# Kernel optimization log

Hardware: AMD Instinct MI355X
Metric: run time of the kernel (lower is better)

The kernel has to match this reference:

```python
import jax, jax.numpy as jnp
import numpy as np

CHUNKS = 4
QMAX = 127.0

def fake_quant_int8(t):
    # per-tensor amax calibration -> symmetric int8 fake quant with STE
    amax = jnp.max(jnp.abs(t))
    scale = jnp.maximum(amax, 1e-12) / QMAX
    q = jnp.clip(jnp.round(t / scale), -128.0, 127.0) * scale
    return t + jax.lax.stop_gradient(q - t)

def conv2d(x, w):
    # NCHW x, OIHW w; stride 1, padding 1, dilation 1, groups 1
    return jax.lax.conv_general_dilated(
        x, w, window_strides=(1, 1), padding=((1, 1), (1, 1)),
        dimension_numbers=('NCHW', 'OIHW', 'NCHW'))

def setup_inputs() -> dict:
    key = jax.random.key(0)
    k1, k2, k3 = jax.random.split(key, 3)
    x = jax.random.normal(k1, (8, 256, 128, 128), dtype=jnp.float32)
    weight = jax.random.normal(k2, (512, 256, 3, 3), dtype=jnp.float32) * 0.05
    bias_data = jax.random.normal(k3, (512,), dtype=jnp.float32)
    return {'x': x, 'weight': weight, 'bias_data': bias_data}

def reference(x, weight, bias_data):
    # seg_mode='weight', opt_type='default': input quantized once,
    # weight chunked along out_channels, each chunk quantized separately.
    xq = fake_quant_int8(x)
    out_ch = weight.shape[0]
    csize = out_ch // CHUNKS
    outs = []
    for i in range(CHUNKS):
        w_chunk = weight[i * csize:(i + 1) * csize]
        wq = fake_quant_int8(w_chunk)
        outs.append(conv2d(xq, wq))
    res = jnp.concatenate(outs, axis=1)  # [B, out_ch, H, W]
    return res + bias_data[None, :, None, None]
```

## Files before the change

kernel.cpp:

```cpp
#include <hip/hip_runtime.h>
#include <hip/hip_bf16.h>


typedef int i32x4 __attribute__((ext_vector_type(4)));

__device__ __forceinline__ void llds16(const void* g, void* l) {
    __builtin_amdgcn_global_load_lds(
        (const __attribute__((address_space(1))) void*)g,
        (__attribute__((address_space(3))) void*)l,
        16, 0, 0);
}

__device__ __forceinline__ float f4max(float4 v) {
    return fmaxf(fmaxf(fabsf(v.x), fabsf(v.y)), fmaxf(fabsf(v.z), fabsf(v.w)));
}

__global__ __launch_bounds__(256) void k_amax(const float4* __restrict__ x,
                                              const float4* __restrict__ w4,
                                              float* __restrict__ part) {
    __shared__ float red[4];
    int t = threadIdx.x;
    float m = 0.f;
    if (blockIdx.x < 2048) {
        int tid = blockIdx.x * 256 + t;
        float4 v[16];
#pragma unroll
        for (int k = 0; k < 16; ++k)
            v[k] = x[(size_t)tid + (size_t)k * 524288];
#pragma unroll
        for (int k = 0; k < 16; ++k) m = fmaxf(m, f4max(v[k]));
    } else {
        int b = blockIdx.x - 2048;
        int chunk = b / 288;
        int tid = (b - chunk * 288) * 256 + t;
        m = f4max(w4[(size_t)chunk * 73728 + tid]);
    }
    for (int off = 32; off > 0; off >>= 1) m = fmaxf(m, __shfl_xor(m, off, 64));
    if ((t & 63) == 0) red[t >> 6] = m;
    __syncthreads();
    if (t == 0)
        part[blockIdx.x] = fmaxf(fmaxf(red[0], red[1]), fmaxf(red[2], red[3]));
}

__global__ __launch_bounds__(256) void k_amax2(const float* __restrict__ part,
                                               unsigned* __restrict__ amaxb) {
    __shared__ float red[4];
    int t = threadIdx.x;
    float m = 0.f;
#pragma unroll
    for (int k = 0; k < 8; ++k) m = fmaxf(m, part[t + k * 256]);
    for (int off = 32; off > 0; off >>= 1) m = fmaxf(m, __shfl_xor(m, off, 64));
    if ((t & 63) == 0) red[t >> 6] = m;
    __syncthreads();
    if (t == 0)
        amaxb[0] = __float_as_uint(fmaxf(fmaxf(red[0], red[1]), fmaxf(red[2], red[3])));
    int c = t >> 6, l = t & 63;
    float wm = 0.f;
#pragma unroll
    for (int k = 0; k < 5; ++k) {
        int i = l + k * 64;
        if (i < 288) wm = fmaxf(wm, part[2048 + c * 288 + i]);
    }
    for (int off = 32; off > 0; off >>= 1) wm = fmaxf(wm, __shfl_xor(wm, off, 64));
    if (l == 0) amaxb[1 + c] = __float_as_uint(wm);
}

__global__ __launch_bounds__(256) void k_quant_x(const float* __restrict__ x,
                                                 signed char* __restrict__ qx,
                                                 const unsigned* __restrict__ amaxb) {
    float inv = 127.0f / fmaxf(__uint_as_float(amaxb[0]), 1e-12f);
    int row = blockIdx.x;
    int n = row >> 7, h = row & 127;
    int t = threadIdx.x;
    int w4 = t & 31, cg = t >> 5;
    const float* base = x + (size_t)n * 256 * 16384 + (size_t)h * 128 + w4 * 4;
#pragma unroll
    for (int pp = 0; pp < 2; ++pp) {
        int c0 = pp * 128 + cg * 16;
        float4 v[16];
#pragma unroll
        for (int j = 0; j < 16; ++j)
            v[j] = *(const float4*)(base + (size_t)(c0 + j) * 16384);
#pragma unroll
        for (int i = 0; i < 4; ++i) {
            unsigned wds[4];
#pragma unroll
            for (int jg = 0; jg < 4; ++jg) {
                unsigned u = 0;
#pragma unroll
                for (int jj = 0; jj < 4; ++jj) {
                    float f = (&v[jg * 4 + jj].x)[i];
                    int q = (int)fminf(fmaxf(rintf(f * inv), -128.f), 127.f);
                    u |= ((unsigned)(q & 255)) << (8 * jj);
                }
                wds[jg] = u;
            }
            *(uint4*)&qx[(size_t)row * 32768 + (size_t)(w4 * 4 + i) * 256 + c0] =
                make_uint4(wds[0], wds[1], wds[2], wds[3]);
        }
    }
}

__global__ void k_quant_w(const float* __restrict__ wsrc, signed char* __restrict__ qw,
                          const unsigned* __restrict__ amaxb) {
    int idx = blockIdx.x * 256 + threadIdx.x;
    int oc = idx >> 8, c = idx & 255;
    float inv = 127.0f / fmaxf(__uint_as_float(amaxb[1 + (oc >> 7)]), 1e-12f);
    const float* src = wsrc + (size_t)idx * 9;
    float v[9];
#pragma unroll
    for (int rs = 0; rs < 9; ++rs) v[rs] = src[rs];
#pragma unroll
    for (int rs = 0; rs < 9; ++rs) {
        float qf = fminf(fmaxf(rintf(v[rs] * inv), -128.f), 127.f);
        qw[((size_t)(rs * 512 + oc)) * 256 + c] = (signed char)(int)qf;
    }
}

__global__ __launch_bounds__(256, 2) void k_conv(
    const signed char* __restrict__ qx, const signed char* __restrict__ qw,
    const signed char* __restrict__ zb, const unsigned* __restrict__ amaxb,
    const float* __restrict__ bias, float* __restrict__ out) {
    __shared__ __align__(16) signed char xs[4 * 8320];
    __shared__ __align__(16) signed char wt[3 * 128 * 64];
    int orig = blockIdx.x;
    int wgid = (orig & 7) * 256 + (orig >> 3);
    int rowpair = wgid >> 2, ocg = wgid & 3;
    int n = rowpair >> 6;
    int h0 = (rowpair & 63) * 2;
    int t = threadIdx.x, wid = t >> 6, lane = t & 63;
    int lp = lane & 15, hi = lane >> 4;
    int rowsel = wid >> 1, whalf = wid & 1;

    i32x4 acc[8][4] = {};

    auto stageX = [&](int cb) {
#pragma unroll
        for (int i = 0; i < 9; ++i) {
            int idx = t + i * 256;
            if (idx < 2080) {
                int rowk = idx / 520;
                int j = idx - rowk * 520;
                int wr = j >> 2, q4 = j & 3;
                int wg = wr - 1;
                int hh = h0 - 1 + rowk;
                int q4s = q4 ^ ((wr >> 1) & 3);
                const signed char* src = (hh >= 0 && hh < 128 && wg >= 0 && wg < 128)
                    ? qx + (size_t)(n * 128 + hh) * 32768 + wg * 256 + cb * 64 + q4s * 16
                    : zb;
                llds16(src, xs + (size_t)(i * 256 + wid * 64) * 16);
            }
        }
    };
    auto stageW = [&](int cb, int r) {
#pragma unroll
        for (int i = 0; i < 6; ++i) {
            int idx = t + i * 256;
            int s = idx >> 9, rem = idx & 511;
            int oc = rem >> 2, q4 = rem & 3;
            int q4s = q4 ^ ((oc >> 1) & 3);
            const signed char* src = qw
                + (size_t)((r * 3 + s) * 512 + ocg * 128 + oc) * 256 + cb * 64 + q4s * 16;
            llds16(src, wt + (size_t)(i * 256 + wid * 64) * 16);
        }
    };
    auto rdA = [&](int s, i32x4* a) {
#pragma unroll
        for (int mf = 0; mf < 8; ++mf) {
            int ocr = mf * 16 + lp;
            a[mf] = *(const i32x4*)&wt[s * 8192 + ocr * 64
                                       + ((hi ^ ((ocr >> 1) & 3)) << 4)];
        }
    };
    auto rdB = [&](int s, int rowk, i32x4* b) {
#pragma unroll
        for (int nf = 0; nf < 4; ++nf) {
            int slot = whalf * 64 + nf * 16 + lp + s;
            b[nf] = *(const i32x4*)&xs[rowk * 8320 + slot * 64
                                       + ((hi ^ ((slot >> 1) & 3)) << 4)];
        }
    };
    auto domm = [&](i32x4* a, i32x4* b) {
        __builtin_amdgcn_s_setprio(1);
#pragma unroll
        for (int mf = 0; mf < 8; ++mf)
#pragma unroll
            for (int nf = 0; nf < 4; ++nf)
                acc[mf][nf] = __builtin_amdgcn_mfma_i32_16x16x64_i8(
                    a[mf], b[nf], acc[mf][nf], 0, 0, 0);
        __builtin_amdgcn_s_setprio(0);
    };

    for (int cb = 0; cb < 4; ++cb) {
#pragma unroll
        for (int r = 0; r < 3; ++r) {
            if (r == 0) stageX(cb);
            stageW(cb, r);
            __syncthreads();
            int rowk = r + rowsel;
            i32x4 aA[8], bA[4], aB[8], bB[4];
            rdA(0, aA); rdB(0, rowk, bA);
            rdA(1, aB); rdB(1, rowk, bB);
            domm(aA, bA);
            rdA(2, aA); rdB(2, rowk, bA);
            domm(aB, bB);
            domm(aA, bA);
            __syncthreads();
        }
    }

    float sx = fmaxf(__uint_as_float(amaxb[0]), 1e-12f) / 127.0f;
    float sw = fmaxf(__uint_as_float(amaxb[1 + ocg]), 1e-12f) / 127.0f;
    float sc = sx * sw;
    int h = h0 + rowsel;
#pragma unroll
    for (int mf = 0; mf < 8; ++mf)
#pragma unroll
        for (int nf = 0; nf < 4; ++nf)
#pragma unroll
            for (int j = 0; j < 4; ++j) {
                int oc = ocg * 128 + mf * 16 + hi * 4 + j;
                int px = whalf * 64 + nf * 16 + lp;
                out[((size_t)(n * 512 + oc) * 128 + h) * 128 + px] =
                    (float)acc[mf][nf][j] * sc + bias[oc];
            }
}

extern "C" void kernel_launch(void* const* d_in, const int* in_sizes, int n_in,
                              void* d_out, int out_size, void* d_ws, size_t ws_size,
                              hipStream_t stream) {
    const float* x    = (const float*)d_in[0];
    const float* wgt  = (const float*)d_in[1];
    const float* bias = (const float*)d_in[2];
    float* out = (float*)d_out;

    unsigned* amaxb = (unsigned*)d_ws;
    float* part = (float*)((char*)d_ws + 256);
    signed char* qx = (signed char*)d_ws + 16384;
    signed char* qw = (signed char*)d_ws + 16384 + 33554432;
    const signed char* zb = (const signed char*)d_ws + 64;

    hipMemsetAsync(d_ws, 0, 256, stream);

    k_amax<<<3200, 256, 0, stream>>>((const float4*)x, (const float4*)wgt, part);
    k_amax2<<<1, 256, 0, stream>>>(part, amaxb);
    k_quant_x<<<1024, 256, 0, stream>>>(x, qx, amaxb);
    k_quant_w<<<512, 256, 0, stream>>>(wgt, qw, amaxb);
    k_conv<<<dim3(2048), 256, 0, stream>>>(qx, qw, zb, amaxb, bias, out);
}
```

Baseline: 273.7 us.

## Double-buffer LDS staging and overlap next-phase loads with MFMA compute

Splits the X and W LDS tiles into two buffers and issues the global-to-LDS loads for the next (channel-block, row) phase before computing the current one, using explicit vmcnt waits and raw barriers. X staging is simplified so that zero padding columns are written once up front instead of being loaded from a zero buffer. Occupancy drops from two to one workgroup per CU to fit the doubled LDS, and the s_setprio hints are removed. The hand-tuned vmcnt counts must match the number of outstanding loads exactly, or the kernel reads stale data.

Result: faster. 262.9 us (-3.9%).

```diff
diff --git a/kernel.cpp b/kernel.cpp
--- a/kernel.cpp
+++ b/kernel.cpp
@@ -13,6 +13,12 @@
 
 __device__ __forceinline__ float f4max(float4 v) {
     return fmaxf(fmaxf(fabsf(v.x), fabsf(v.y)), fmaxf(fabsf(v.z), fabsf(v.w)));
+}
+
+__device__ __forceinline__ void barrier_f() {
+    asm volatile("" ::: "memory");
+    __builtin_amdgcn_s_barrier();
+    asm volatile("" ::: "memory");
 }
 
 __global__ __launch_bounds__(256) void k_amax(const float4* __restrict__ x,
@@ -117,12 +123,12 @@
     }
 }
 
-__global__ __launch_bounds__(256, 2) void k_conv(
+__global__ __launch_bounds__(256, 1) void k_conv(
     const signed char* __restrict__ qx, const signed char* __restrict__ qw,
     const signed char* __restrict__ zb, const unsigned* __restrict__ amaxb,
     const float* __restrict__ bias, float* __restrict__ out) {
-    __shared__ __align__(16) signed char xs[4 * 8320];
-    __shared__ __align__(16) signed char wt[3 * 128 * 64];
+    __shared__ __align__(16) signed char xs2[2][4 * 8320];
+    __shared__ __align__(16) signed char wt2[2][3 * 8192];
     int orig = blockIdx.x;
     int wgid = (orig & 7) * 256 + (orig >> 3);
     int rowpair = wgid >> 2, ocg = wgid & 3;
@@ -134,25 +140,23 @@
 
     i32x4 acc[8][4] = {};
 
-    auto stageX = [&](int cb) {
-#pragma unroll
-        for (int i = 0; i < 9; ++i) {
-            int idx = t + i * 256;
-            if (idx < 2080) {
-                int rowk = idx / 520;
-                int j = idx - rowk * 520;
-                int wr = j >> 2, q4 = j & 3;
-                int wg = wr - 1;
-                int hh = h0 - 1 + rowk;
-                int q4s = q4 ^ ((wr >> 1) & 3);
-                const signed char* src = (hh >= 0 && hh < 128 && wg >= 0 && wg < 128)
-                    ? qx + (size_t)(n * 128 + hh) * 32768 + wg * 256 + cb * 64 + q4s * 16
+    auto stageX = [&](int cb, int buf) {
+#pragma unroll
+        for (int rowk = 0; rowk < 4; ++rowk) {
+            int hh = h0 - 1 + rowk;
+#pragma unroll
+            for (int i = 0; i < 2; ++i) {
+                int idx = t + i * 256;
+                int w = idx >> 2, q4 = idx & 3;
+                int q4s = q4 ^ (((w + 1) >> 1) & 3);
+                const signed char* src = (hh >= 0 && hh < 128)
+                    ? qx + (size_t)(n * 128 + hh) * 32768 + w * 256 + cb * 64 + q4s * 16
                     : zb;
-                llds16(src, xs + (size_t)(i * 256 + wid * 64) * 16);
+                llds16(src, &xs2[buf][0] + rowk * 8320 + 64 + (size_t)idx * 16);
             }
         }
     };
-    auto stageW = [&](int cb, int r) {
+    auto stageW = [&](int cb, int r, int buf) {
 #pragma unroll
         for (int i = 0; i < 6; ++i) {
             int idx = t + i * 256;
@@ -161,53 +165,70 @@
             int q4s = q4 ^ ((oc >> 1) & 3);
             const signed char* src = qw
                 + (size_t)((r * 3 + s) * 512 + ocg * 128 + oc) * 256 + cb * 64 + q4s * 16;
-            llds16(src, wt + (size_t)(i * 256 + wid * 64) * 16);
-        }
-    };
-    auto rdA = [&](int s, i32x4* a) {
+            llds16(src, &wt2[buf][0] + (size_t)idx * 16);
+        }
+    };
+    auto rdA = [&](int wb, int s, i32x4* a) {
 #pragma unroll
         for (int mf = 0; mf < 8; ++mf) {
             int ocr = mf * 16 + lp;
-            a[mf] = *(const i32x4*)&wt[s * 8192 + ocr * 64
-                                       + ((hi ^ ((ocr >> 1) & 3)) << 4)];
-        }
-    };
-    auto rdB = [&](int s, int rowk, i32x4* b) {
+            a[mf] = *(const i32x4*)&wt2[wb][s * 8192 + ocr * 64
+                                           + ((hi ^ ((ocr >> 1) & 3)) << 4)];
+        }
+    };
+    auto rdB = [&](int xb, int s, int rowk, i32x4* b) {
 #pragma unroll
         for (int nf = 0; nf < 4; ++nf) {
             int slot = whalf * 64 + nf * 16 + lp + s;
-            b[nf] = *(const i32x4*)&xs[rowk * 8320 + slot * 64
-                                       + ((hi ^ ((slot >> 1) & 3)) << 4)];
+            b[nf] = *(const i32x4*)&xs2[xb][rowk * 8320 + slot * 64
+                                            + ((hi ^ ((slot >> 1) & 3)) << 4)];
         }
     };
     auto domm = [&](i32x4* a, i32x4* b) {
-        __builtin_amdgcn_s_setprio(1);
 #pragma unroll
         for (int mf = 0; mf < 8; ++mf)
 #pragma unroll
             for (int nf = 0; nf < 4; ++nf)
                 acc[mf][nf] = __builtin_amdgcn_mfma_i32_16x16x64_i8(
                     a[mf], b[nf], acc[mf][nf], 0, 0, 0);
-        __builtin_amdgcn_s_setprio(0);
-    };
-
-    for (int cb = 0; cb < 4; ++cb) {
-#pragma unroll
-        for (int r = 0; r < 3; ++r) {
-            if (r == 0) stageX(cb);
-            stageW(cb, r);
-            __syncthreads();
-            int rowk = r + rowsel;
-            i32x4 aA[8], bA[4], aB[8], bB[4];
-            rdA(0, aA); rdB(0, rowk, bA);
-            rdA(1, aB); rdB(1, rowk, bB);
-            domm(aA, bA);
-            rdA(2, aA); rdB(2, rowk, bA);
-            domm(aB, bB);
-            domm(aA, bA);
-            __syncthreads();
-        }
-    }
+    };
+
+    if (t < 64) {
+        int buf = t >> 5, rem = t & 31;
+        int row = rem >> 3, side = (rem >> 2) & 1, q = rem & 3;
+        *(i32x4*)&xs2[buf][row * 8320 + (side ? 129 : 0) * 64 + q * 16] =
+            i32x4{0, 0, 0, 0};
+    }
+    stageX(0, 0);
+    stageW(0, 0, 0);
+    asm volatile("s_waitcnt lgkmcnt(0)" ::: "memory");
+
+#define PHASE(P, NW)                                                          \
+    {                                                                         \
+        constexpr int cb_ = (P) / 3, r_ = (P) % 3;                            \
+        barrier_f();                        \
+        if ((P) < 11) {                                                       \
+            constexpr int cbn = ((P) + 1) / 3, rn = ((P) + 1) % 3;            \
+            if (rn == 0) stageX(cbn, cbn & 1);                                \
+            stageW(cbn, rn, ((P) + 1) & 1);                                   \
+        }                                                                     \
+        asm volatile("s_waitcnt vmcnt(" #NW ")" ::: "memory");                \
+        barrier_f();                      \
+        {                                                                     \
+            const int rowk = r_ + rowsel;                                     \
+            i32x4 aA[8], bA[4], aB[8], bB[4];                                 \
+            rdA((P) & 1, 0, aA); rdB(cb_ & 1, 0, rowk, bA);                   \
+            rdA((P) & 1, 1, aB); rdB(cb_ & 1, 1, rowk, bB);                   \
+            domm(aA, bA);                       \
+            rdA((P) & 1, 2, aA); rdB(cb_ & 1, 2, rowk, bA);                   \
+            domm(aB, bB);                       \
+            domm(aA, bA);                                            \
+        }                                                                     \
+    }
+
+    PHASE(0, 6)  PHASE(1, 6)  PHASE(2, 14) PHASE(3, 6)  PHASE(4, 6)  PHASE(5, 14)
+    PHASE(6, 6)  PHASE(7, 6)  PHASE(8, 14) PHASE(9, 6)  PHASE(10, 6) PHASE(11, 0)
+#undef PHASE
 
     float sx = fmaxf(__uint_as_float(amaxb[0]), 1e-12f) / 127.0f;
     float sw = fmaxf(__uint_as_float(amaxb[1 + ocg]), 1e-12f) / 127.0f;
```

## Load activation fragments directly from global memory instead of staging in LDS

Applied to the files above, without the earlier changes.

Removes the LDS staging buffer for the quantized input tile and has each lane load its B-operand fragments straight from global memory, with zero-padding handled by pointing out-of-range lanes at a zero buffer. This cuts LDS usage, which may allow higher occupancy, and drops the X staging copy. It also reorders loads so that the third shift's fragments are fetched while MFMAs on the first run, and it removes the s_setprio hints. The cost is redundant global and L2 traffic, since neighbouring rows and shifts reload overlapping data, and the MFMAs may stall on global-load latency.

Measured after the change: 383.7 us. 1.4x slower.

```diff
diff --git a/kernel.cpp b/kernel.cpp
--- a/kernel.cpp
+++ b/kernel.cpp
@@ -121,7 +121,6 @@
     const signed char* __restrict__ qx, const signed char* __restrict__ qw,
     const signed char* __restrict__ zb, const unsigned* __restrict__ amaxb,
     const float* __restrict__ bias, float* __restrict__ out) {
-    __shared__ __align__(16) signed char xs[4 * 8320];
     __shared__ __align__(16) signed char wt[3 * 128 * 64];
     int orig = blockIdx.x;
     int wgid = (orig & 7) * 256 + (orig >> 3);
@@ -134,24 +133,6 @@
 
     i32x4 acc[8][4] = {};
 
-    auto stageX = [&](int cb) {
-#pragma unroll
-        for (int i = 0; i < 9; ++i) {
-            int idx = t + i * 256;
-            if (idx < 2080) {
-                int rowk = idx / 520;
-                int j = idx - rowk * 520;
-                int wr = j >> 2, q4 = j & 3;
-                int wg = wr - 1;
-                int hh = h0 - 1 + rowk;
-                int q4s = q4 ^ ((wr >> 1) & 3);
-                const signed char* src = (hh >= 0 && hh < 128 && wg >= 0 && wg < 128)
-                    ? qx + (size_t)(n * 128 + hh) * 32768 + wg * 256 + cb * 64 + q4s * 16
-                    : zb;
-                llds16(src, xs + (size_t)(i * 256 + wid * 64) * 16);
-            }
-        }
-    };
     auto stageW = [&](int cb, int r) {
 #pragma unroll
         for (int i = 0; i < 6; ++i) {
@@ -172,39 +153,44 @@
                                        + ((hi ^ ((ocr >> 1) & 3)) << 4)];
         }
     };
-    auto rdB = [&](int s, int rowk, i32x4* b) {
+    auto ldB = [&](int cb, int rowk, int s, i32x4* b) {
+        int hh = h0 - 1 + rowk;
+        bool rok = (hh >= 0) && (hh < 128);
+        const signed char* rowbase =
+            qx + (size_t)(n * 128 + (rok ? hh : 0)) * 32768 + cb * 64 + hi * 16;
 #pragma unroll
         for (int nf = 0; nf < 4; ++nf) {
-            int slot = whalf * 64 + nf * 16 + lp + s;
-            b[nf] = *(const i32x4*)&xs[rowk * 8320 + slot * 64
-                                       + ((hi ^ ((slot >> 1) & 3)) << 4)];
+            int w = whalf * 64 + nf * 16 + lp + s - 1;
+            bool ok = rok && (w >= 0) && (w < 128);
+            const signed char* src = ok ? rowbase + (size_t)w * 256 : zb;
+            b[nf] = *(const i32x4*)src;
         }
     };
     auto domm = [&](i32x4* a, i32x4* b) {
-        __builtin_amdgcn_s_setprio(1);
 #pragma unroll
         for (int mf = 0; mf < 8; ++mf)
 #pragma unroll
             for (int nf = 0; nf < 4; ++nf)
                 acc[mf][nf] = __builtin_amdgcn_mfma_i32_16x16x64_i8(
                     a[mf], b[nf], acc[mf][nf], 0, 0, 0);
-        __builtin_amdgcn_s_setprio(0);
     };
 
     for (int cb = 0; cb < 4; ++cb) {
 #pragma unroll
         for (int r = 0; r < 3; ++r) {
-            if (r == 0) stageX(cb);
+            int rowk = r + rowsel;
+            i32x4 a[8], b0[4], b1[4];
+            ldB(cb, rowk, 0, b0);
+            ldB(cb, rowk, 1, b1);
             stageW(cb, r);
             __syncthreads();
-            int rowk = r + rowsel;
-            i32x4 aA[8], bA[4], aB[8], bB[4];
-            rdA(0, aA); rdB(0, rowk, bA);
-            rdA(1, aB); rdB(1, rowk, bB);
-            domm(aA, bA);
-            rdA(2, aA); rdB(2, rowk, bA);
-            domm(aB, bB);
-            domm(aA, bA);
+            rdA(0, a);
+            domm(a, b0);
+            ldB(cb, rowk, 2, b0);
+            rdA(1, a);
+            domm(a, b1);
+            rdA(2, a);
+            domm(a, b0);
             __syncthreads();
         }
     }
```
